# Optimization experiments

Hardware: AMD Instinct MI355X
Metric: run time of the kernel (lower is better)

The kernel has to match this reference:

```python
import jax, jax.numpy as jnp
import numpy as np

N, L, DS, DP, H, A, Q, V = 1, 512, 384, 256, 12, 16, 4, 8
SHID = H * (DP + A + 3 * V + V)  # 3648
WC = float(np.sqrt(2.0 / (9.0 * Q)))
WL = float(np.sqrt(1.0 / 3.0))
EPS = 1e-5


def quat2rot(q):
    # q: (..., 3) partial quaternion (w fixed to 1, then normalized) -> (..., 3, 3)
    ones = jnp.ones(q.shape[:-1] + (1,), q.dtype)
    qf = jnp.concatenate([ones, q], axis=-1)
    qf = qf / jnp.linalg.norm(qf, axis=-1, keepdims=True)
    w, x, y, z = qf[..., 0], qf[..., 1], qf[..., 2], qf[..., 3]
    r0 = jnp.stack([1 - 2 * (y * y + z * z), 2 * (x * y - w * z), 2 * (x * z + w * y)], -1)
    r1 = jnp.stack([2 * (x * y + w * z), 1 - 2 * (x * x + z * z), 2 * (y * z - w * x)], -1)
    r2 = jnp.stack([2 * (x * z - w * y), 2 * (y * z + w * x), 1 - 2 * (x * x + y * y)], -1)
    return jnp.stack([r0, r1, r2], axis=-2)


def layer_norm(x, g, b):
    m = x.mean(-1, keepdims=True)
    v = ((x - m) ** 2).mean(-1, keepdims=True)
    return (x - m) / jnp.sqrt(v + EPS) * g + b


def setup_inputs() -> dict:
    key = jax.random.key(0)
    ks = jax.random.split(key, 24)
    w = lambda k, shape, s=0.02: (jax.random.normal(k, shape, jnp.float32) * s)
    return {
        'sfea': jax.random.normal(ks[0], (N, L, DS), jnp.float32),
        'pfea': jax.random.normal(ks[1], (N, L, L, DP), jnp.float32),
        'quat': jax.random.normal(ks[2], (N, L, 3), jnp.float32) * 0.1,
        'trsl': jax.random.normal(ks[3], (N, L, 3), jnp.float32),
        'Wq': w(ks[4], (DS, H * A)), 'Wk': w(ks[5], (DS, H * A)), 'Wv': w(ks[6], (DS, H * A)),
        'Wqp': w(ks[7], (DS, H * Q * 3)), 'Wkp': w(ks[8], (DS, H * Q * 3)), 'Wvp': w(ks[9], (DS, H * V * 3)),
        'Wb': w(ks[10], (DP, H)),
        'scale': jnp.ones((H,), jnp.float32),
        'Ws': w(ks[11], (SHID, DS)), 'bs': jnp.zeros((DS,), jnp.float32),
        'W1': w(ks[12], (DS, DS)), 'b1': jnp.zeros((DS,), jnp.float32),
        'W2': w(ks[13], (DS, DS)), 'b2': jnp.zeros((DS,), jnp.float32),
        'W3': w(ks[14], (DS, DS)), 'b3': jnp.zeros((DS,), jnp.float32),
        'g1': jnp.ones((DS,), jnp.float32), 'be1': jnp.zeros((DS,), jnp.float32),
        'g2': jnp.ones((DS,), jnp.float32), 'be2': jnp.zeros((DS,), jnp.float32),
    }


def reference(sfea, pfea, quat, trsl, Wq, Wk, Wv, Wqp, Wkp, Wvp, Wb, scale, Ws, bs,
              W1, b1, W2, b2, W3, b3, g1, be1, g2, be2):
    n, l = sfea.shape[0], sfea.shape[1]
    # projections
    q = (sfea @ Wq).reshape(n, l, H, A)
    k = (sfea @ Wk).reshape(n, l, H, A)
    v = (sfea @ Wv).reshape(n, l, H, A)
    qp = (sfea @ Wqp).reshape(n, l, H, Q, 3)
    kp = (sfea @ Wkp).reshape(n, l, H, Q, 3)
    vp = (sfea @ Wvp).reshape(n, l, H, V, 3)
    b = jnp.einsum('nijp,ph->nijh', pfea, Wb)
    # local frames
    rot = quat2rot(quat)  # (n, l, 3, 3)
    t = trsl[:, :, None, None, :]
    qp_g = jnp.einsum('nlij,nlhqj->nlhqi', rot, qp) + t
    kp_g = jnp.einsum('nlij,nlhqj->nlhqi', rot, kp) + t
    vp_g = jnp.einsum('nlij,nlhvj->nlhvi', rot, vp) + t
    # attention logits
    qk = jnp.einsum('nihd,njhd->nijh', q, k) / np.sqrt(A)
    diff = qp_g[:, :, None] - kp_g[:, None]  # (n, i, j, h, q, 3)
    d2 = jnp.sum(diff * diff, axis=(-1, -2))  # (n, i, j, h)
    qkp = (WC * jax.nn.softplus(scale) / 2.0) * d2
    a = jax.nn.softmax(WL * (qk + b - qkp), axis=2)  # (n, i, j, h)
    # weighted sums (einsum avoids huge broadcast intermediates)
    op = jnp.einsum('nijh,nijp->nihp', a, pfea)
    ov = jnp.einsum('nijh,njhd->nihd', a, v)
    ovp_g = jnp.einsum('nijh,njhvc->nihvc', a, vp_g)
    # map back into local frame: R^T (x - t)
    ovp = jnp.einsum('nlji,nlhvj->nlhvi', rot, ovp_g - t)
    ovp_norm = jnp.sqrt(jnp.sum(ovp * ovp, axis=-1))  # (n, l, h, v)
    shid = jnp.concatenate([op, ov, ovp.reshape(n, l, H, V * 3), ovp_norm], axis=-1)
    shid = shid.reshape(n, l, SHID)
    # output projection + residual, post-LN, MLP, post-LN (v1 path, p_drop=0)
    s = sfea + shid @ Ws + bs
    s = layer_norm(s, g1, be1)
    h = jax.nn.relu(s @ W1 + b1)
    h = jax.nn.relu(h @ W2 + b2)
    s = s + (h @ W3 + b3)
    s = layer_norm(s, g2, be2)
    return s
```

## Files before the change

### kernel.cpp

```cpp
#include <hip/hip_runtime.h>
#include <cstddef>

typedef __attribute__((ext_vector_type(8))) short short8;
typedef __attribute__((ext_vector_type(4))) float f32x4;

#define WC_CONST 0.2357022603955158f
#define WL_CONST 0.5773502691896258f

__device__ __forceinline__ unsigned short rne_bf16(float f) {
  unsigned int u = __float_as_uint(f);
  u += 0x7fffu + ((u >> 16) & 1u);
  return (unsigned short)(u >> 16);
}

__global__ __launch_bounds__(256) void concat_w_kernel(
    const float* __restrict__ Wq, const float* __restrict__ Wk, const float* __restrict__ Wv,
    const float* __restrict__ Wqp, const float* __restrict__ Wkp, const float* __restrict__ Wvp,
    float* __restrict__ Wcat) {
  int idx = blockIdx.x * 256 + threadIdx.x;
  if (idx >= 384 * 1152) return;
  int k = idx / 1152, c = idx % 1152;
  float v;
  if (c < 192)       v = Wq [k*192 + c];
  else if (c < 384)  v = Wk [k*192 + (c-192)];
  else if (c < 576)  v = Wv [k*192 + (c-384)];
  else if (c < 720)  v = Wqp[k*144 + (c-576)];
  else if (c < 864)  v = Wkp[k*144 + (c-720)];
  else               v = Wvp[k*288 + (c-864)];
  Wcat[idx] = v;
}

__global__ __launch_bounds__(256) void gemm64_kernel(
    const float* __restrict__ Amat, const float* __restrict__ Bmat, float* __restrict__ Cp,
    int M, int N, int K, int ksl) {
  __shared__ float As[16][68];
  __shared__ float Bs[16][68];
  int t = threadIdx.x;
  int bn = blockIdx.x, bm = blockIdx.y, bz = blockIdx.z;
  int k0 = bz * ksl;
  int tr = t >> 4, tc = t & 15;
  int lm = t >> 2, lk4 = (t & 3) << 2;
  int lkb = t >> 4, lnq = (t & 15) << 2;
  const float* Ab = Amat + (size_t)(bm*64 + lm) * K;
  const float* Bb = Bmat + bn*64 + lnq;
  float acc[4][4];
  #pragma unroll
  for (int a2 = 0; a2 < 4; a2++)
    #pragma unroll
    for (int b2 = 0; b2 < 4; b2++) acc[a2][b2] = 0.f;

  for (int k = k0; k < k0 + ksl; k += 16) {
    float4 av = *(const float4*)(Ab + k + lk4);
    float4 bv = *(const float4*)(Bb + (size_t)(k + lkb) * N);
    As[lk4+0][lm] = av.x; As[lk4+1][lm] = av.y; As[lk4+2][lm] = av.z; As[lk4+3][lm] = av.w;
    *(float4*)&Bs[lkb][lnq] = bv;
    __syncthreads();
    #pragma unroll
    for (int kk = 0; kk < 16; kk++) {
      float4 a4 = *(const float4*)&As[kk][tr << 2];
      float4 b4 = *(const float4*)&Bs[kk][tc << 2];
      float ar[4] = {a4.x, a4.y, a4.z, a4.w};
      float br[4] = {b4.x, b4.y, b4.z, b4.w};
      #pragma unroll
      for (int a2 = 0; a2 < 4; a2++)
        #pragma unroll
        for (int b2 = 0; b2 < 4; b2++) acc[a2][b2] += ar[a2] * br[b2];
    }
    __syncthreads();
  }
  float* Cb = Cp + (size_t)bz * M * N + (size_t)(bm*64 + (tr << 2)) * N + bn*64 + (tc << 2);
  #pragma unroll
  for (int r = 0; r < 4; r++) {
    float4 o = {acc[r][0], acc[r][1], acc[r][2], acc[r][3]};
    *(float4*)(Cb + (size_t)r * N) = o;
  }
}

__global__ __launch_bounds__(256) void reduce_kernel(
    const float* __restrict__ Cp, float* __restrict__ out, const float* __restrict__ bias,
    int relu, int MN, int N, int sk) {
  int idx = blockIdx.x * 256 + threadIdx.x;
  if (idx >= MN) return;
  float s = 0.f;
  for (int z = 0; z < sk; z++) s += Cp[(size_t)z * MN + idx];
  if (bias) s += bias[idx % N];
  if (relu) s = fmaxf(s, 0.f);
  out[idx] = s;
}

__global__ __launch_bounds__(256) void gemm32_kernel(
    const float* __restrict__ Amat, const float* __restrict__ Bmat,
    const float* __restrict__ bias,
    float* __restrict__ C, int M, int N, int K, int relu) {
  __shared__ float As[16][34];
  __shared__ float Bs[16][34];
  int t = threadIdx.x;
  int bn = blockIdx.x, bm = blockIdx.y;
  int tr = t >> 4, tc = t & 15;
  int lm = t >> 3, lk2 = (t & 7) << 1;
  int lkb = t >> 4, ln2 = (t & 15) << 1;
  const float* Ab = Amat + (size_t)(bm*32 + lm) * K;
  const float* Bb = Bmat + bn*32 + ln2;
  float a00=0.f, a01=0.f, a10=0.f, a11=0.f;
  for (int k = 0; k < K; k += 16) {
    float2 av = *(const float2*)(Ab + k + lk2);
    float2 bv = *(const float2*)(Bb + (size_t)(k + lkb) * N);
    As[lk2][lm] = av.x; As[lk2+1][lm] = av.y;
    *(float2*)&Bs[lkb][ln2] = bv;
    __syncthreads();
    #pragma unroll
    for (int kk = 0; kk < 16; kk++) {
      float2 a2 = *(const float2*)&As[kk][tr << 1];
      float2 b2 = *(const float2*)&Bs[kk][tc << 1];
      a00 += a2.x*b2.x; a01 += a2.x*b2.y; a10 += a2.y*b2.x; a11 += a2.y*b2.y;
    }
    __syncthreads();
  }
  int r0 = bm*32 + (tr << 1), c0 = bn*32 + (tc << 1);
  float bb0 = bias ? bias[c0] : 0.f, bb1 = bias ? bias[c0+1] : 0.f;
  float o00 = a00 + bb0, o01 = a01 + bb1, o10 = a10 + bb0, o11 = a11 + bb1;
  if (relu) { o00=fmaxf(o00,0.f); o01=fmaxf(o01,0.f); o10=fmaxf(o10,0.f); o11=fmaxf(o11,0.f); }
  float2 w0 = {o00, o01}, w1 = {o10, o11};
  *(float2*)(C + (size_t)r0*N + c0) = w0;
  *(float2*)(C + (size_t)(r0+1)*N + c0) = w1;
}

__global__ __launch_bounds__(64) void frames_kernel(
    const float* __restrict__ proj, const float* __restrict__ quat, const float* __restrict__ trsl,
    float* __restrict__ rotb, float* __restrict__ qpg, float* __restrict__ kpg,
    float* __restrict__ vpg) {
  int i = blockIdx.x, t = threadIdx.x;
  float q0 = quat[i*3+0], q1 = quat[i*3+1], q2 = quat[i*3+2];
  float inv = rsqrtf(1.f + q0*q0 + q1*q1 + q2*q2);
  float w = inv, x = q0*inv, y = q1*inv, z = q2*inv;
  float R00 = 1.f - 2.f*(y*y + z*z), R01 = 2.f*(x*y - w*z), R02 = 2.f*(x*z + w*y);
  float R10 = 2.f*(x*y + w*z), R11 = 1.f - 2.f*(x*x + z*z), R12 = 2.f*(y*z - w*x);
  float R20 = 2.f*(x*z - w*y), R21 = 2.f*(y*z + w*x), R22 = 1.f - 2.f*(x*x + y*y);
  float t0 = trsl[i*3+0], t1 = trsl[i*3+1], t2 = trsl[i*3+2];
  if (t == 0) {
    float* rb = rotb + i*9;
    rb[0]=R00; rb[1]=R01; rb[2]=R02; rb[3]=R10; rb[4]=R11; rb[5]=R12; rb[6]=R20; rb[7]=R21; rb[8]=R22;
  }
  for (int pt = t; pt < 192; pt += 64) {
    const float* src; float* dst;
    if (pt < 48)      { src = proj + i*1152 + 576 + pt*3;        dst = qpg + i*144 + pt*3; }
    else if (pt < 96) { src = proj + i*1152 + 720 + (pt-48)*3;   dst = kpg + i*144 + (pt-48)*3; }
    else              { src = proj + i*1152 + 864 + (pt-96)*3;   dst = vpg + i*288 + (pt-96)*3; }
    float p0 = src[0], p1 = src[1], p2 = src[2];
    dst[0] = R00*p0 + R01*p1 + R02*p2 + t0;
    dst[1] = R10*p0 + R11*p1 + R12*p2 + t1;
    dst[2] = R20*p0 + R21*p1 + R22*p2 + t2;
  }
}

__global__ __launch_bounds__(256) void bgemm_kernel(
    const float* __restrict__ pfea, const float* __restrict__ Wb, float* __restrict__ bmat) {
  __shared__ short wbf[8][64][8];
  int t = threadIdx.x;
  for (int s = t; s < 512; s += 256) {
    int ks = s >> 6, l = s & 63;
    int col = l & 15, kb = ks * 32 + ((l >> 4) << 3);
    #pragma unroll
    for (int j = 0; j < 8; j++)
      wbf[ks][l][j] = (col < 12) ? (short)rne_bf16(Wb[(kb + j) * 12 + col]) : (short)0;
  }
  __syncthreads();
  int wv = t >> 6, lane = t & 63;
  int wglob = blockIdx.x * 4 + wv;
  int row = lane & 15, kq = lane >> 4;
  for (int it = 0; it < 4; it++) {
    int tile = wglob * 4 + it;
    size_t p0 = (size_t)tile * 16;
    const float* Ab = pfea + (p0 + row) * 256 + kq * 8;
    f32x4 acc = {0.f, 0.f, 0.f, 0.f};
    #pragma unroll
    for (int ks = 0; ks < 8; ks++) {
      float4 f0 = *(const float4*)(Ab + ks * 32);
      float4 f1 = *(const float4*)(Ab + ks * 32 + 4);
      short8 af;
      af[0] = (short)rne_bf16(f0.x); af[1] = (short)rne_bf16(f0.y);
      af[2] = (short)rne_bf16(f0.z); af[3] = (short)rne_bf16(f0.w);
      af[4] = (short)rne_bf16(f1.x); af[5] = (short)rne_bf16(f1.y);
      af[6] = (short)rne_bf16(f1.z); af[7] = (short)rne_bf16(f1.w);
      short8 bfv = *(const short8*)(&wbf[ks][lane][0]);
      acc = __builtin_amdgcn_mfma_f32_16x16x32_bf16(af, bfv, acc, 0, 0, 0);
    }
    int col = lane & 15;
    if (col < 12) {
      #pragma unroll
      for (int r = 0; r < 4; r++) {
        size_t pr = p0 + kq * 4 + r;
        bmat[pr * 12 + col] = acc[r];
      }
    }
  }
}

__device__ __forceinline__ float lt1_val(
    const float* __restrict__ proj, const float* __restrict__ kpg,
    const float* qs_, const float* qps_, float coef, int jg, int h) {
  const float4* kr = (const float4*)(proj + (size_t)jg*1152 + 192 + h*16);
  const float4* qr = (const float4*)(qs_ + h*16);
  float qk = 0.f;
  #pragma unroll
  for (int m = 0; m < 4; m++) {
    float4 kv = kr[m], qv = qr[m];
    qk += qv.x*kv.x + qv.y*kv.y + qv.z*kv.z + qv.w*kv.w;
  }
  const float4* kpr = (const float4*)(kpg + (size_t)jg*144 + h*12);
  const float4* qpr = (const float4*)(qps_ + h*12);
  float d2 = 0.f;
  #pragma unroll
  for (int m = 0; m < 3; m++) {
    float4 kv = kpr[m], qv = qpr[m];
    float dx = qv.x-kv.x, dy = qv.y-kv.y, dz = qv.z-kv.z, dw = qv.w-kv.w;
    d2 += dx*dx + dy*dy + dz*dz + dw*dw;
  }
  return qk*0.25f - coef*d2;
}

__global__ __launch_bounds__(768) void attn5_kernel(
    const float* __restrict__ proj, const float* __restrict__ qpg,
    const float* __restrict__ kpg, const float* __restrict__ vpg,
    const float* __restrict__ pfea, const float* __restrict__ bmat,
    const float* __restrict__ rotb, const float* __restrict__ trsl,
    const float* __restrict__ scale, float* __restrict__ shid) {
  __shared__ float Lws[512][12];
  __shared__ __align__(16) float4 opred[12][2][64];
  __shared__ __align__(16) float qs[12][16];
  __shared__ __align__(16) float qps[12][12];
  __shared__ float coefs[12], sh_inv[12], rot_s[9];
  __shared__ float ovpg_l[12][24];

  int i = blockIdx.x, t = threadIdx.x;
  int w = t >> 6, lane = t & 63;

  for (int idx = t; idx < 192; idx += 768) qs[idx >> 4][idx & 15] = proj[i*1152 + idx];
  for (int idx = t; idx < 144; idx += 768) qps[idx / 12][idx % 12] = qpg[i*144 + idx];
  if (t < 12) coefs[t] = WC_CONST * 0.5f * log1pf(__expf(scale[t]));
  if (t < 9)  rot_s[t] = rotb[i*9 + t];
  __syncthreads();

  #pragma unroll
  for (int r = 0; r < 8; r++) {
    int idx = t + r * 768;
    int j = idx / 12, h = idx - j * 12;
    float lb = lt1_val(proj, kpg, &qs[0][0], &qps[0][0], coefs[h], j, h);
    Lws[j][h] = __expf(WL_CONST * (lb + bmat[(size_t)i * 6144 + idx]));
  }
  __syncthreads();

  {
    float sacc = 0.f;
    #pragma unroll
    for (int r2 = 0; r2 < 8; r2++) sacc += Lws[lane + 64 * r2][w];
    #pragma unroll
    for (int off = 32; off >= 1; off >>= 1) sacc += __shfl_xor(sacc, off);
    if (lane == 0) sh_inv[w] = 1.0f / sacc;
  }

  float4 opacc[12];
  #pragma unroll
  for (int h = 0; h < 12; h++) { opacc[h].x=0.f; opacc[h].y=0.f; opacc[h].z=0.f; opacc[h].w=0.f; }
  float accv[3] = {0.f, 0.f, 0.f};
  float accvp[5] = {0.f, 0.f, 0.f, 0.f, 0.f};
  int hv0 = lane >> 4, hv1 = 4 + (lane >> 4), hv2 = 8 + (lane >> 4);
  int hp0 = lane / 24, hp1 = (lane + 64) / 24, hp2 = (lane + 128) / 24,
      hp3 = (lane + 192) / 24, hp4 = (lane + 256) / 24;

  const float* pf = pfea + (size_t)i * 131072 + (lane << 2);
  int nrows = (w < 8) ? 43 : 42;

  float4 pv0 = *(const float4*)(pf + (size_t)w * 256);
  float4 pv1 = *(const float4*)(pf + (size_t)(w + 12) * 256);

  for (int r = 0; r < nrows; r++) {
    int j = w + 12 * r;
    float4 pv = pv0;
    pv0 = pv1;
    int jn = w + 12 * (r + 2); if (jn > 511) jn = 511;
    pv1 = *(const float4*)(pf + (size_t)jn * 256);

    const float* vrow  = proj + (size_t)j * 1152 + 384 + lane;
    const float* vprow = vpg  + (size_t)j * 288 + lane;
    float vv0 = vrow[0],  vv1 = vrow[64],  vv2 = vrow[128];
    float vp0 = vprow[0], vp1 = vprow[64], vp2 = vprow[128], vp3 = vprow[192];
    float vp4 = (lane < 32) ? vprow[256] : 0.f;

    const float4* lwp = (const float4*)&Lws[j][0];
    float4 lw0 = lwp[0], lw1 = lwp[1], lw2 = lwp[2];
    float wv[12] = {lw0.x, lw0.y, lw0.z, lw0.w,
                    lw1.x, lw1.y, lw1.z, lw1.w,
                    lw2.x, lw2.y, lw2.z, lw2.w};
    #pragma unroll
    for (int h = 0; h < 12; h++) {
      opacc[h].x += wv[h] * pv.x; opacc[h].y += wv[h] * pv.y;
      opacc[h].z += wv[h] * pv.z; opacc[h].w += wv[h] * pv.w;
    }
    accv[0] += wv[hv0] * vv0; accv[1] += wv[hv1] * vv1; accv[2] += wv[hv2] * vv2;
    accvp[0] += wv[hp0] * vp0; accvp[1] += wv[hp1] * vp1;
    accvp[2] += wv[hp2] * vp2; accvp[3] += wv[hp3] * vp3;
    if (lane < 32) accvp[4] += wv[hp4] * vp4;
  }
  __syncthreads();

  #pragma unroll
  for (int g = 0; g < 6; g++) {
    opred[w][0][lane] = opacc[2*g + 0];
    opred[w][1][lane] = opacc[2*g + 1];
    __syncthreads();
    if (t < 128) {
      int hh = t >> 6, ll = t & 63;
      float4 s = {0.f, 0.f, 0.f, 0.f};
      #pragma unroll
      for (int w2 = 0; w2 < 12; w2++) {
        float4 v = opred[w2][hh][ll];
        s.x += v.x; s.y += v.y; s.z += v.z; s.w += v.w;
      }
      int h = 2*g + hh;
      float isv = sh_inv[h];
      float4 o = {s.x*isv, s.y*isv, s.z*isv, s.w*isv};
      *(float4*)(shid + (size_t)i * 3648 + h * 304 + (ll << 2)) = o;
    }
    __syncthreads();
  }

  float* fred = (float*)&opred[0][0][0];
  fred[w * 192 + lane]       = accv[0];
  fred[w * 192 + 64 + lane]  = accv[1];
  fred[w * 192 + 128 + lane] = accv[2];
  __syncthreads();
  if (t < 192) {
    int h = t >> 4;
    float s = 0.f;
    #pragma unroll
    for (int w2 = 0; w2 < 12; w2++) s += fred[w2 * 192 + t];
    shid[(size_t)i * 3648 + h * 304 + 256 + (t & 15)] = s * sh_inv[h];
  }
  __syncthreads();

  #pragma unroll
  for (int k = 0; k < 4; k++) fred[w * 288 + 64 * k + lane] = accvp[k];
  if (lane < 32) fred[w * 288 + 256 + lane] = accvp[4];
  __syncthreads();
  if (t < 288) {
    int h = t / 24;
    float s = 0.f;
    #pragma unroll
    for (int w2 = 0; w2 < 12; w2++) s += fred[w2 * 288 + t];
    ovpg_l[h][t - h * 24] = s * sh_inv[h];
  }
  __syncthreads();

  if (t < 96) {
    int h = t >> 3, vv = t & 7;
    float x = ovpg_l[h][vv*3+0] - trsl[i*3+0];
    float y = ovpg_l[h][vv*3+1] - trsl[i*3+1];
    float z = ovpg_l[h][vv*3+2] - trsl[i*3+2];
    float o0 = rot_s[0]*x + rot_s[3]*y + rot_s[6]*z;
    float o1 = rot_s[1]*x + rot_s[4]*y + rot_s[7]*z;
    float o2 = rot_s[2]*x + rot_s[5]*y + rot_s[8]*z;
    float* so = shid + (size_t)i*3648 + h*304 + 272 + vv*3;
    so[0] = o0; so[1] = o1; so[2] = o2;
    shid[(size_t)i*3648 + h*304 + 296 + vv] = sqrtf(o0*o0 + o1*o1 + o2*o2);
  }
}

__global__ __launch_bounds__(384) void ln384_kernel(
    const float* __restrict__ resid, const float* __restrict__ C, const float* __restrict__ bias,
    const float* __restrict__ g, const float* __restrict__ be, float* __restrict__ out) {
  int i = blockIdx.x, t = threadIdx.x;
  __shared__ float red[6];
  float x = resid[(size_t)i*384 + t] + C[(size_t)i*384 + t] + bias[t];
  float s = x;
  #pragma unroll
  for (int off = 32; off >= 1; off >>= 1) s += __shfl_xor(s, off);
  if ((t & 63) == 0) red[t >> 6] = s;
  __syncthreads();
  float m = (red[0]+red[1]+red[2]+red[3]+red[4]+red[5]) * (1.f/384.f);
  __syncthreads();
  float d = x - m;
  float v = d * d;
  #pragma unroll
  for (int off = 32; off >= 1; off >>= 1) v += __shfl_xor(v, off);
  if ((t & 63) == 0) red[t >> 6] = v;
  __syncthreads();
  float var = (red[0]+red[1]+red[2]+red[3]+red[4]+red[5]) * (1.f/384.f);
  out[(size_t)i*384 + t] = d * rsqrtf(var + 1e-5f) * g[t] + be[t];
}

extern "C" void kernel_launch(void* const* d_in, const int* in_sizes, int n_in,
                              void* d_out, int out_size, void* d_ws, size_t ws_size,
                              hipStream_t stream) {
  const float* sfea = (const float*)d_in[0];
  const float* pfea = (const float*)d_in[1];
  const float* quat = (const float*)d_in[2];
  const float* trsl = (const float*)d_in[3];
  const float* Wq   = (const float*)d_in[4];
  const float* Wk   = (const float*)d_in[5];
  const float* Wv   = (const float*)d_in[6];
  const float* Wqp  = (const float*)d_in[7];
  const float* Wkp  = (const float*)d_in[8];
  const float* Wvp  = (const float*)d_in[9];
  const float* Wb   = (const float*)d_in[10];
  const float* scale= (const float*)d_in[11];
  const float* Wsm  = (const float*)d_in[12];
  const float* bs   = (const float*)d_in[13];
  const float* W1   = (const float*)d_in[14];
  const float* b1   = (const float*)d_in[15];
  const float* W2   = (const float*)d_in[16];
  const float* b2   = (const float*)d_in[17];
  const float* W3   = (const float*)d_in[18];
  const float* b3   = (const float*)d_in[19];
  const float* g1   = (const float*)d_in[20];
  const float* be1  = (const float*)d_in[21];
  const float* g2   = (const float*)d_in[22];
  const float* be2  = (const float*)d_in[23];
  float* out = (float*)d_out;
  float* wsf = (float*)d_ws;

  float* Wcat = wsf;
  float* proj = Wcat + 442368;
  float* rotb = proj + 589824;
  float* qpg  = rotb + 4608;
  float* kpg  = qpg + 73728;
  float* vpg  = kpg + 73728;
  float* bmat = vpg + 147456;
  float* shid = bmat + 3145728;
  float* cpart= shid + 1867776;
  float* C1   = cpart + 1179648;
  float* s1   = C1 + 196608;
  float* h1   = s1 + 196608;
  float* h2   = h1 + 196608;
  float* C3   = h2 + 196608;

  concat_w_kernel<<<1728, 256, 0, stream>>>(Wq, Wk, Wv, Wqp, Wkp, Wvp, Wcat);
  gemm64_kernel<<<dim3(18, 8, 1), 256, 0, stream>>>(sfea, Wcat, proj, 512, 1152, 384, 384);
  frames_kernel<<<512, 64, 0, stream>>>(proj, quat, trsl, rotb, qpg, kpg, vpg);
  bgemm_kernel<<<1024, 256, 0, stream>>>(pfea, Wb, bmat);
  attn5_kernel<<<512, 768, 0, stream>>>(proj, qpg, kpg, vpg, pfea, bmat, rotb, trsl, scale, shid);

  gemm64_kernel<<<dim3(6, 8, 6), 256, 0, stream>>>(shid, Wsm, cpart, 512, 384, 3648, 608);
  reduce_kernel<<<768, 256, 0, stream>>>(cpart, C1, nullptr, 0, 196608, 384, 6);
  ln384_kernel<<<512, 384, 0, stream>>>(sfea, C1, bs, g1, be1, s1);

  gemm32_kernel<<<dim3(12, 16), 256, 0, stream>>>(s1, W1, b1, h1, 512, 384, 384, 1);
  gemm32_kernel<<<dim3(12, 16), 256, 0, stream>>>(h1, W2, b2, h2, 512, 384, 384, 1);
  gemm32_kernel<<<dim3(12, 16), 256, 0, stream>>>(h2, W3, nullptr, C3, 512, 384, 384, 0);
  ln384_kernel<<<512, 384, 0, stream>>>(s1, C3, b3, g2, be2, out);
}
```

Before: 332.3 us.

## Widen attention block to 16 waves with contiguous rows and float4 value loads

The attention kernel now runs 1024 threads (16 waves) instead of 768. Each wave walks a contiguous run of 32 key rows rather than a stride-12 interleave. The v and vp gathers change from several scalar loads per row to float4 loads with a two-row-ahead prefetch, and pfea gets a three-row-ahead prefetch. The cross-wave reductions widen to 16 partials and use float4 stores. This aims to raise memory-level parallelism and cut load instruction count, at the cost of more shared memory for partials. The launch-bounds hint of 4 blocks per CU may push the compiler to limit registers and spill the 48-float accumulator set.

```diff
diff --git a/kernel.cpp b/kernel.cpp
--- a/kernel.cpp
+++ b/kernel.cpp
@@ -219,14 +219,14 @@
   return qk*0.25f - coef*d2;
 }
 
-__global__ __launch_bounds__(768) void attn5_kernel(
+__global__ __launch_bounds__(1024, 4) void attn6_kernel(
     const float* __restrict__ proj, const float* __restrict__ qpg,
     const float* __restrict__ kpg, const float* __restrict__ vpg,
     const float* __restrict__ pfea, const float* __restrict__ bmat,
     const float* __restrict__ rotb, const float* __restrict__ trsl,
     const float* __restrict__ scale, float* __restrict__ shid) {
   __shared__ float Lws[512][12];
-  __shared__ __align__(16) float4 opred[12][2][64];
+  __shared__ __align__(16) float4 opred[16][2][64];
   __shared__ __align__(16) float qs[12][16];
   __shared__ __align__(16) float qps[12][12];
   __shared__ float coefs[12], sh_inv[12], rot_s[9];
@@ -235,22 +235,22 @@
   int i = blockIdx.x, t = threadIdx.x;
   int w = t >> 6, lane = t & 63;
 
-  for (int idx = t; idx < 192; idx += 768) qs[idx >> 4][idx & 15] = proj[i*1152 + idx];
-  for (int idx = t; idx < 144; idx += 768) qps[idx / 12][idx % 12] = qpg[i*144 + idx];
+  for (int idx = t; idx < 192; idx += 1024) qs[idx >> 4][idx & 15] = proj[i*1152 + idx];
+  for (int idx = t; idx < 144; idx += 1024) qps[idx / 12][idx % 12] = qpg[i*144 + idx];
   if (t < 12) coefs[t] = WC_CONST * 0.5f * log1pf(__expf(scale[t]));
   if (t < 9)  rot_s[t] = rotb[i*9 + t];
   __syncthreads();
 
   #pragma unroll
-  for (int r = 0; r < 8; r++) {
-    int idx = t + r * 768;
+  for (int r = 0; r < 6; r++) {
+    int idx = t + r * 1024;
     int j = idx / 12, h = idx - j * 12;
     float lb = lt1_val(proj, kpg, &qs[0][0], &qps[0][0], coefs[h], j, h);
     Lws[j][h] = __expf(WL_CONST * (lb + bmat[(size_t)i * 6144 + idx]));
   }
   __syncthreads();
 
-  {
+  if (w < 12) {
     float sacc = 0.f;
     #pragma unroll
     for (int r2 = 0; r2 < 8; r2++) sacc += Lws[lane + 64 * r2][w];
@@ -262,30 +262,40 @@
   float4 opacc[12];
   #pragma unroll
   for (int h = 0; h < 12; h++) { opacc[h].x=0.f; opacc[h].y=0.f; opacc[h].z=0.f; opacc[h].w=0.f; }
-  float accv[3] = {0.f, 0.f, 0.f};
-  float accvp[5] = {0.f, 0.f, 0.f, 0.f, 0.f};
-  int hv0 = lane >> 4, hv1 = 4 + (lane >> 4), hv2 = 8 + (lane >> 4);
-  int hp0 = lane / 24, hp1 = (lane + 64) / 24, hp2 = (lane + 128) / 24,
-      hp3 = (lane + 192) / 24, hp4 = (lane + 256) / 24;
-
-  const float* pf = pfea + (size_t)i * 131072 + (lane << 2);
-  int nrows = (w < 8) ? 43 : 42;
-
-  float4 pv0 = *(const float4*)(pf + (size_t)w * 256);
-  float4 pv1 = *(const float4*)(pf + (size_t)(w + 12) * 256);
-
-  for (int r = 0; r < nrows; r++) {
-    int j = w + 12 * r;
-    float4 pv = pv0;
-    pv0 = pv1;
-    int jn = w + 12 * (r + 2); if (jn > 511) jn = 511;
-    pv1 = *(const float4*)(pf + (size_t)jn * 256);
-
-    const float* vrow  = proj + (size_t)j * 1152 + 384 + lane;
-    const float* vprow = vpg  + (size_t)j * 288 + lane;
-    float vv0 = vrow[0],  vv1 = vrow[64],  vv2 = vrow[128];
-    float vp0 = vprow[0], vp1 = vprow[64], vp2 = vprow[128], vp3 = vprow[192];
-    float vp4 = (lane < 32) ? vprow[256] : 0.f;
+  float4 accv  = {0.f, 0.f, 0.f, 0.f};
+  float4 accvp = {0.f, 0.f, 0.f, 0.f};
+  float4 accvt = {0.f, 0.f, 0.f, 0.f};
+  int hva = (lane < 48) ? (lane >> 2) : 0;
+  int hpa = lane / 6;
+  int hpt = (lane < 2) ? 10 : 11;
+
+  int j0 = w * 32;
+  const float* pfp  = pfea + (size_t)i * 131072 + (size_t)j0 * 256 + (lane << 2);
+  const float* vbp  = proj + (size_t)j0 * 1152 + 384 + (lane << 2);
+  const float* vpbp = vpg  + (size_t)j0 * 288 + (lane << 2);
+  const float* vptp = vpg  + (size_t)j0 * 288 + 256 + (lane << 2);
+
+  float4 pvA = *(const float4*)(pfp);
+  float4 pvB = *(const float4*)(pfp + 256);
+  float4 pvC = *(const float4*)(pfp + 512);
+  float4 vA  = *(const float4*)(vbp);
+  float4 vB  = *(const float4*)(vbp + 1152);
+  float4 vpA = *(const float4*)(vpbp);
+  float4 vpB = *(const float4*)(vpbp + 288);
+  float4 vtA = (lane < 8) ? *(const float4*)(vptp)       : float4{0,0,0,0};
+  float4 vtB = (lane < 8) ? *(const float4*)(vptp + 288) : float4{0,0,0,0};
+
+  for (int r = 0; r < 32; r++) {
+    int j = j0 + r;
+    float4 pv = pvA, vv = vA, vp = vpA, vt = vtA;
+    pvA = pvB; pvB = pvC;
+    int rp3 = (r + 3 < 32) ? (r + 3) : 31;
+    pvC = *(const float4*)(pfp + (size_t)rp3 * 256);
+    vA = vB; vpA = vpB; vtA = vtB;
+    int rp2 = (r + 2 < 32) ? (r + 2) : 31;
+    vB  = *(const float4*)(vbp  + (size_t)rp2 * 1152);
+    vpB = *(const float4*)(vpbp + (size_t)rp2 * 288);
+    if (lane < 8) vtB = *(const float4*)(vptp + (size_t)rp2 * 288);
 
     const float4* lwp = (const float4*)&Lws[j][0];
     float4 lw0 = lwp[0], lw1 = lwp[1], lw2 = lwp[2];
@@ -297,10 +307,12 @@
       opacc[h].x += wv[h] * pv.x; opacc[h].y += wv[h] * pv.y;
       opacc[h].z += wv[h] * pv.z; opacc[h].w += wv[h] * pv.w;
     }
-    accv[0] += wv[hv0] * vv0; accv[1] += wv[hv1] * vv1; accv[2] += wv[hv2] * vv2;
-    accvp[0] += wv[hp0] * vp0; accvp[1] += wv[hp1] * vp1;
-    accvp[2] += wv[hp2] * vp2; accvp[3] += wv[hp3] * vp3;
-    if (lane < 32) accvp[4] += wv[hp4] * vp4;
+    float wva = wv[hva];
+    accv.x += wva * vv.x; accv.y += wva * vv.y; accv.z += wva * vv.z; accv.w += wva * vv.w;
+    float wvp = wv[hpa];
+    accvp.x += wvp * vp.x; accvp.y += wvp * vp.y; accvp.z += wvp * vp.z; accvp.w += wvp * vp.w;
+    float wvt = wv[hpt];
+    accvt.x += wvt * vt.x; accvt.y += wvt * vt.y; accvt.z += wvt * vt.z; accvt.w += wvt * vt.w;
   }
   __syncthreads();
 
@@ -313,7 +325,7 @@
       int hh = t >> 6, ll = t & 63;
       float4 s = {0.f, 0.f, 0.f, 0.f};
       #pragma unroll
-      for (int w2 = 0; w2 < 12; w2++) {
+      for (int w2 = 0; w2 < 16; w2++) {
         float4 v = opred[w2][hh][ll];
         s.x += v.x; s.y += v.y; s.z += v.z; s.w += v.w;
       }
@@ -326,28 +338,26 @@
   }
 
   float* fred = (float*)&opred[0][0][0];
-  fred[w * 192 + lane]       = accv[0];
-  fred[w * 192 + 64 + lane]  = accv[1];
-  fred[w * 192 + 128 + lane] = accv[2];
+  float4* fred4 = (float4*)fred;
+  if (lane < 48) fred4[w * 48 + lane] = accv;
   __syncthreads();
   if (t < 192) {
     int h = t >> 4;
     float s = 0.f;
     #pragma unroll
-    for (int w2 = 0; w2 < 12; w2++) s += fred[w2 * 192 + t];
+    for (int w2 = 0; w2 < 16; w2++) s += fred[w2 * 192 + t];
     shid[(size_t)i * 3648 + h * 304 + 256 + (t & 15)] = s * sh_inv[h];
   }
   __syncthreads();
 
-  #pragma unroll
-  for (int k = 0; k < 4; k++) fred[w * 288 + 64 * k + lane] = accvp[k];
-  if (lane < 32) fred[w * 288 + 256 + lane] = accvp[4];
+  fred4[w * 72 + lane] = accvp;
+  if (lane < 8) fred4[w * 72 + 64 + lane] = accvt;
   __syncthreads();
   if (t < 288) {
     int h = t / 24;
     float s = 0.f;
     #pragma unroll
-    for (int w2 = 0; w2 < 12; w2++) s += fred[w2 * 288 + t];
+    for (int w2 = 0; w2 < 16; w2++) s += fred[w2 * 288 + t];
     ovpg_l[h][t - h * 24] = s * sh_inv[h];
   }
   __syncthreads();
@@ -438,7 +448,7 @@
   gemm64_kernel<<<dim3(18, 8, 1), 256, 0, stream>>>(sfea, Wcat, proj, 512, 1152, 384, 384);
   frames_kernel<<<512, 64, 0, stream>>>(proj, quat, trsl, rotb, qpg, kpg, vpg);
   bgemm_kernel<<<1024, 256, 0, stream>>>(pfea, Wb, bmat);
-  attn5_kernel<<<512, 768, 0, stream>>>(proj, qpg, kpg, vpg, pfea, bmat, rotb, trsl, scale, shid);
+  attn6_kernel<<<512, 1024, 0, stream>>>(proj, qpg, kpg, vpg, pfea, bmat, rotb, trsl, scale, shid);
 
   gemm64_kernel<<<dim3(6, 8, 6), 256, 0, stream>>>(shid, Wsm, cpart, 512, 384, 3648, 608);
   reduce_kernel<<<768, 256, 0, stream>>>(cpart, C1, nullptr, 0, 196608, 384, 6);
```

Result: slower. 385.7 us (+16.1%).

## Split value aggregation into separate kernel with transposed weight and value layouts

Applied to the files above, without the earlier changes.

The attention kernel now only computes softmax weights and the pfea-weighted sum, with each wave pair handling half the heads over a strided set of rows. The per-head weights are written out in a transposed layout. A new kernel computes the v and vp weighted sums as coalesced dot products over transposed value arrays, then applies the inverse frame transform. The bias matrix is also stored transposed so each wave reads its head contiguously. This cuts register pressure and scattered loads in the main loop, at the cost of an extra launch and a roughly 12 MB weight round trip through memory.

```diff
diff --git a/kernel.cpp b/kernel.cpp
--- a/kernel.cpp
+++ b/kernel.cpp
@@ -128,7 +128,7 @@
 __global__ __launch_bounds__(64) void frames_kernel(
     const float* __restrict__ proj, const float* __restrict__ quat, const float* __restrict__ trsl,
     float* __restrict__ rotb, float* __restrict__ qpg, float* __restrict__ kpg,
-    float* __restrict__ vpg) {
+    float* __restrict__ vvT) {
   int i = blockIdx.x, t = threadIdx.x;
   float q0 = quat[i*3+0], q1 = quat[i*3+1], q2 = quat[i*3+2];
   float inv = rsqrtf(1.f + q0*q0 + q1*q1 + q2*q2);
@@ -141,20 +141,34 @@
     float* rb = rotb + i*9;
     rb[0]=R00; rb[1]=R01; rb[2]=R02; rb[3]=R10; rb[4]=R11; rb[5]=R12; rb[6]=R20; rb[7]=R21; rb[8]=R22;
   }
-  for (int pt = t; pt < 192; pt += 64) {
+  for (int pt = t; pt < 96; pt += 64) {
     const float* src; float* dst;
-    if (pt < 48)      { src = proj + i*1152 + 576 + pt*3;        dst = qpg + i*144 + pt*3; }
-    else if (pt < 96) { src = proj + i*1152 + 720 + (pt-48)*3;   dst = kpg + i*144 + (pt-48)*3; }
-    else              { src = proj + i*1152 + 864 + (pt-96)*3;   dst = vpg + i*288 + (pt-96)*3; }
+    if (pt < 48) { src = proj + i*1152 + 576 + pt*3;      dst = qpg + i*144 + pt*3; }
+    else         { src = proj + i*1152 + 720 + (pt-48)*3; dst = kpg + i*144 + (pt-48)*3; }
     float p0 = src[0], p1 = src[1], p2 = src[2];
     dst[0] = R00*p0 + R01*p1 + R02*p2 + t0;
     dst[1] = R10*p0 + R11*p1 + R12*p2 + t1;
     dst[2] = R20*p0 + R21*p1 + R22*p2 + t2;
   }
+  for (int o = t; o < 480; o += 64) {
+    float val;
+    if (o < 192) {
+      val = proj[i*1152 + 384 + o];
+    } else {
+      int m = o - 192;
+      int vi = m / 3, c = m - vi * 3;
+      const float* p = proj + i*1152 + 864 + vi*3;
+      float p0 = p[0], p1 = p[1], p2 = p[2];
+      val = (c == 0) ? (R00*p0 + R01*p1 + R02*p2 + t0)
+          : (c == 1) ? (R10*p0 + R11*p1 + R12*p2 + t1)
+                     : (R20*p0 + R21*p1 + R22*p2 + t2);
+    }
+    vvT[(size_t)o * 512 + i] = val;
+  }
 }
 
 __global__ __launch_bounds__(256) void bgemm_kernel(
-    const float* __restrict__ pfea, const float* __restrict__ Wb, float* __restrict__ bmat) {
+    const float* __restrict__ pfea, const float* __restrict__ Wb, float* __restrict__ bmatT) {
   __shared__ short wbf[8][64][8];
   int t = threadIdx.x;
   for (int s = t; s < 512; s += 256) {
@@ -190,7 +204,7 @@
       #pragma unroll
       for (int r = 0; r < 4; r++) {
         size_t pr = p0 + kq * 4 + r;
-        bmat[pr * 12 + col] = acc[r];
+        bmatT[(pr >> 9) * 6144 + (size_t)col * 512 + (pr & 511)] = acc[r];
       }
     }
   }
@@ -219,18 +233,16 @@
   return qk*0.25f - coef*d2;
 }
 
-__global__ __launch_bounds__(768) void attn5_kernel(
+__global__ __launch_bounds__(768) void attn7_kernel(
     const float* __restrict__ proj, const float* __restrict__ qpg,
-    const float* __restrict__ kpg, const float* __restrict__ vpg,
-    const float* __restrict__ pfea, const float* __restrict__ bmat,
-    const float* __restrict__ rotb, const float* __restrict__ trsl,
-    const float* __restrict__ scale, float* __restrict__ shid) {
+    const float* __restrict__ kpg, const float* __restrict__ pfea,
+    const float* __restrict__ bmatT, const float* __restrict__ scale,
+    float* __restrict__ shid, float* __restrict__ wmatT, float* __restrict__ shinv_g) {
   __shared__ float Lws[512][12];
-  __shared__ __align__(16) float4 opred[12][2][64];
+  __shared__ __align__(16) float4 opred[12][64];
   __shared__ __align__(16) float qs[12][16];
   __shared__ __align__(16) float qps[12][12];
-  __shared__ float coefs[12], sh_inv[12], rot_s[9];
-  __shared__ float ovpg_l[12][24];
+  __shared__ float coefs[12], sh_inv[12];
 
   int i = blockIdx.x, t = threadIdx.x;
   int w = t >> 6, lane = t & 63;
@@ -238,117 +250,120 @@
   for (int idx = t; idx < 192; idx += 768) qs[idx >> 4][idx & 15] = proj[i*1152 + idx];
   for (int idx = t; idx < 144; idx += 768) qps[idx / 12][idx % 12] = qpg[i*144 + idx];
   if (t < 12) coefs[t] = WC_CONST * 0.5f * log1pf(__expf(scale[t]));
-  if (t < 9)  rot_s[t] = rotb[i*9 + t];
-  __syncthreads();
-
-  #pragma unroll
-  for (int r = 0; r < 8; r++) {
-    int idx = t + r * 768;
-    int j = idx / 12, h = idx - j * 12;
-    float lb = lt1_val(proj, kpg, &qs[0][0], &qps[0][0], coefs[h], j, h);
-    Lws[j][h] = __expf(WL_CONST * (lb + bmat[(size_t)i * 6144 + idx]));
-  }
-  __syncthreads();
-
+  __syncthreads();
+
+  float wvals[8];
+  {
+    const float* bT = bmatT + (size_t)i * 6144 + (size_t)w * 512;
+    float* wT = wmatT + (size_t)i * 6144 + (size_t)w * 512;
+    float cf = coefs[w];
+    #pragma unroll
+    for (int r = 0; r < 8; r++) {
+      int j = lane + 64 * r;
+      float lb = lt1_val(proj, kpg, &qs[0][0], &qps[0][0], cf, j, w);
+      float val = __expf(WL_CONST * (lb + bT[j]));
+      Lws[j][w] = val;
+      wT[j] = val;
+      wvals[r] = val;
+    }
+  }
   {
     float sacc = 0.f;
     #pragma unroll
-    for (int r2 = 0; r2 < 8; r2++) sacc += Lws[lane + 64 * r2][w];
+    for (int r = 0; r < 8; r++) sacc += wvals[r];
     #pragma unroll
     for (int off = 32; off >= 1; off >>= 1) sacc += __shfl_xor(sacc, off);
-    if (lane == 0) sh_inv[w] = 1.0f / sacc;
-  }
-
-  float4 opacc[12];
-  #pragma unroll
-  for (int h = 0; h < 12; h++) { opacc[h].x=0.f; opacc[h].y=0.f; opacc[h].z=0.f; opacc[h].w=0.f; }
-  float accv[3] = {0.f, 0.f, 0.f};
-  float accvp[5] = {0.f, 0.f, 0.f, 0.f, 0.f};
-  int hv0 = lane >> 4, hv1 = 4 + (lane >> 4), hv2 = 8 + (lane >> 4);
-  int hp0 = lane / 24, hp1 = (lane + 64) / 24, hp2 = (lane + 128) / 24,
-      hp3 = (lane + 192) / 24, hp4 = (lane + 256) / 24;
-
+    if (lane == 0) { sh_inv[w] = 1.0f / sacc; shinv_g[i*12 + w] = 1.0f / sacc; }
+  }
+  __syncthreads();
+
+  int wp = w >> 1, half = w & 1;
+  int nr = (wp < 2) ? 86 : 85;
+  int off0 = half ? 4 : 0, off1 = half ? 8 : 4;
   const float* pf = pfea + (size_t)i * 131072 + (lane << 2);
-  int nrows = (w < 8) ? 43 : 42;
-
-  float4 pv0 = *(const float4*)(pf + (size_t)w * 256);
-  float4 pv1 = *(const float4*)(pf + (size_t)(w + 12) * 256);
-
-  for (int r = 0; r < nrows; r++) {
-    int j = w + 12 * r;
-    float4 pv = pv0;
-    pv0 = pv1;
-    int jn = w + 12 * (r + 2); if (jn > 511) jn = 511;
-    pv1 = *(const float4*)(pf + (size_t)jn * 256);
-
-    const float* vrow  = proj + (size_t)j * 1152 + 384 + lane;
-    const float* vprow = vpg  + (size_t)j * 288 + lane;
-    float vv0 = vrow[0],  vv1 = vrow[64],  vv2 = vrow[128];
-    float vp0 = vprow[0], vp1 = vprow[64], vp2 = vprow[128], vp3 = vprow[192];
-    float vp4 = (lane < 32) ? vprow[256] : 0.f;
-
-    const float4* lwp = (const float4*)&Lws[j][0];
-    float4 lw0 = lwp[0], lw1 = lwp[1], lw2 = lwp[2];
-    float wv[12] = {lw0.x, lw0.y, lw0.z, lw0.w,
-                    lw1.x, lw1.y, lw1.z, lw1.w,
-                    lw2.x, lw2.y, lw2.z, lw2.w};
-    #pragma unroll
-    for (int h = 0; h < 12; h++) {
-      opacc[h].x += wv[h] * pv.x; opacc[h].y += wv[h] * pv.y;
-      opacc[h].z += wv[h] * pv.z; opacc[h].w += wv[h] * pv.w;
-    }
-    accv[0] += wv[hv0] * vv0; accv[1] += wv[hv1] * vv1; accv[2] += wv[hv2] * vv2;
-    accvp[0] += wv[hp0] * vp0; accvp[1] += wv[hp1] * vp1;
-    accvp[2] += wv[hp2] * vp2; accvp[3] += wv[hp3] * vp3;
-    if (lane < 32) accvp[4] += wv[hp4] * vp4;
+
+  float4 opacc[6];
+  #pragma unroll
+  for (int c = 0; c < 6; c++) { opacc[c].x=0.f; opacc[c].y=0.f; opacc[c].z=0.f; opacc[c].w=0.f; }
+
+  float4 pvA = *(const float4*)(pf + (size_t)wp * 256);
+  float4 pvB = *(const float4*)(pf + (size_t)(wp + 6) * 256);
+  float4 pvC = *(const float4*)(pf + (size_t)(wp + 12) * 256);
+  float4 lwA0 = *(const float4*)&Lws[wp][off0];
+  float4 lwA1 = *(const float4*)&Lws[wp][off1];
+
+  for (int r = 0; r < nr; r++) {
+    float4 pv = pvA;
+    pvA = pvB; pvB = pvC;
+    int jn = wp + 6 * (r + 3); if (jn > 511) jn = 511;
+    pvC = *(const float4*)(pf + (size_t)jn * 256);
+
+    float4 lw0 = lwA0, lw1 = lwA1;
+    int jl = wp + 6 * (r + 1); if (jl > 511) jl = wp;
+    lwA0 = *(const float4*)&Lws[jl][off0];
+    lwA1 = *(const float4*)&Lws[jl][off1];
+
+    float wv0, wv1, wv2, wv3, wv4, wv5;
+    if (half == 0) { wv0=lw0.x; wv1=lw0.y; wv2=lw0.z; wv3=lw0.w; wv4=lw1.x; wv5=lw1.y; }
+    else           { wv0=lw0.z; wv1=lw0.w; wv2=lw1.x; wv3=lw1.y; wv4=lw1.z; wv5=lw1.w; }
+
+    opacc[0].x += wv0*pv.x; opacc[0].y += wv0*pv.y; opacc[0].z += wv0*pv.z; opacc[0].w += wv0*pv.w;
+    opacc[1].x += wv1*pv.x; opacc[1].y += wv1*pv.y; opacc[1].z += wv1*pv.z; opacc[1].w += wv1*pv.w;
+    opacc[2].x += wv2*pv.x; opacc[2].y += wv2*pv.y; opacc[2].z += wv2*pv.z; opacc[2].w += wv2*pv.w;
+    opacc[3].x += wv3*pv.x; opacc[3].y += wv3*pv.y; opacc[3].z += wv3*pv.z; opacc[3].w += wv3*pv.w;
+    opacc[4].x += wv4*pv.x; opacc[4].y += wv4*pv.y; opacc[4].z += wv4*pv.z; opacc[4].w += wv4*pv.w;
+    opacc[5].x += wv5*pv.x; opacc[5].y += wv5*pv.y; opacc[5].z += wv5*pv.z; opacc[5].w += wv5*pv.w;
   }
   __syncthreads();
 
   #pragma unroll
   for (int g = 0; g < 6; g++) {
-    opred[w][0][lane] = opacc[2*g + 0];
-    opred[w][1][lane] = opacc[2*g + 1];
+    opred[half * 6 + wp][lane] = opacc[g];
     __syncthreads();
     if (t < 128) {
       int hh = t >> 6, ll = t & 63;
       float4 s = {0.f, 0.f, 0.f, 0.f};
       #pragma unroll
-      for (int w2 = 0; w2 < 12; w2++) {
-        float4 v = opred[w2][hh][ll];
+      for (int w2 = 0; w2 < 6; w2++) {
+        float4 v = opred[hh * 6 + w2][ll];
         s.x += v.x; s.y += v.y; s.z += v.z; s.w += v.w;
       }
-      int h = 2*g + hh;
+      int h = g + 6 * hh;
       float isv = sh_inv[h];
       float4 o = {s.x*isv, s.y*isv, s.z*isv, s.w*isv};
       *(float4*)(shid + (size_t)i * 3648 + h * 304 + (ll << 2)) = o;
     }
     __syncthreads();
   }
-
-  float* fred = (float*)&opred[0][0][0];
-  fred[w * 192 + lane]       = accv[0];
-  fred[w * 192 + 64 + lane]  = accv[1];
-  fred[w * 192 + 128 + lane] = accv[2];
-  __syncthreads();
-  if (t < 192) {
-    int h = t >> 4;
-    float s = 0.f;
-    #pragma unroll
-    for (int w2 = 0; w2 < 12; w2++) s += fred[w2 * 192 + t];
-    shid[(size_t)i * 3648 + h * 304 + 256 + (t & 15)] = s * sh_inv[h];
-  }
-  __syncthreads();
-
-  #pragma unroll
-  for (int k = 0; k < 4; k++) fred[w * 288 + 64 * k + lane] = accvp[k];
-  if (lane < 32) fred[w * 288 + 256 + lane] = accvp[4];
-  __syncthreads();
-  if (t < 288) {
-    int h = t / 24;
-    float s = 0.f;
-    #pragma unroll
-    for (int w2 = 0; w2 < 12; w2++) s += fred[w2 * 288 + t];
-    ovpg_l[h][t - h * 24] = s * sh_inv[h];
+}
+
+__global__ __launch_bounds__(512) void ovph_kernel(
+    const float* __restrict__ wmatT, const float* __restrict__ vvT,
+    const float* __restrict__ shinv_g, const float* __restrict__ rotb,
+    const float* __restrict__ trsl, float* __restrict__ shid) {
+  __shared__ float ovpg_l[12][24];
+  __shared__ float sh_inv[12], rot_s[9];
+  int i = blockIdx.x, t = threadIdx.x;
+  int w = t >> 6, lane = t & 63;
+  if (t < 12) sh_inv[t] = shinv_g[i*12 + t];
+  if (t >= 16 && t < 25) rot_s[t - 16] = rotb[i*9 + (t - 16)];
+  __syncthreads();
+
+  const float* wbase = wmatT + (size_t)i * 6144;
+  for (int o = w * 60; o < w * 60 + 60; o++) {
+    int h = (o < 192) ? (o >> 4) : ((o - 192) / 24);
+    const float* wrow = wbase + (size_t)h * 512 + lane;
+    const float* vrow = vvT + (size_t)o * 512 + lane;
+    float acc = 0.f;
+    #pragma unroll
+    for (int k = 0; k < 8; k++) acc += wrow[64*k] * vrow[64*k];
+    #pragma unroll
+    for (int off = 32; off >= 1; off >>= 1) acc += __shfl_xor(acc, off);
+    if (lane == 0) {
+      float val = acc * sh_inv[h];
+      if (o < 192) shid[(size_t)i * 3648 + h * 304 + 256 + (o & 15)] = val;
+      else         ovpg_l[h][(o - 192) - h * 24] = val;
+    }
   }
   __syncthreads();
 
@@ -419,26 +434,30 @@
   float* out = (float*)d_out;
   float* wsf = (float*)d_ws;
 
-  float* Wcat = wsf;
-  float* proj = Wcat + 442368;
-  float* rotb = proj + 589824;
-  float* qpg  = rotb + 4608;
-  float* kpg  = qpg + 73728;
-  float* vpg  = kpg + 73728;
-  float* bmat = vpg + 147456;
-  float* shid = bmat + 3145728;
-  float* cpart= shid + 1867776;
-  float* C1   = cpart + 1179648;
-  float* s1   = C1 + 196608;
-  float* h1   = s1 + 196608;
-  float* h2   = h1 + 196608;
-  float* C3   = h2 + 196608;
+  float* Wcat  = wsf;
+  float* proj  = Wcat + 442368;
+  float* rotb  = proj + 589824;
+  float* qpg   = rotb + 4608;
+  float* kpg   = qpg + 73728;
+  float* vvT   = kpg + 73728;
+  float* big   = vvT + 245760;
+  float* wmatT = big + 3145728;
+  float* shinv = wmatT + 3145728;
+  float* shid  = shinv + 6144;
+  float* C1    = shid + 1867776;
+  float* s1    = C1 + 196608;
+  float* h1    = s1 + 196608;
+  float* h2    = h1 + 196608;
+  float* C3    = h2 + 196608;
+  float* bmatT = big;
+  float* cpart = big;
 
   concat_w_kernel<<<1728, 256, 0, stream>>>(Wq, Wk, Wv, Wqp, Wkp, Wvp, Wcat);
   gemm64_kernel<<<dim3(18, 8, 1), 256, 0, stream>>>(sfea, Wcat, proj, 512, 1152, 384, 384);
-  frames_kernel<<<512, 64, 0, stream>>>(proj, quat, trsl, rotb, qpg, kpg, vpg);
-  bgemm_kernel<<<1024, 256, 0, stream>>>(pfea, Wb, bmat);
-  attn5_kernel<<<512, 768, 0, stream>>>(proj, qpg, kpg, vpg, pfea, bmat, rotb, trsl, scale, shid);
+  frames_kernel<<<512, 64, 0, stream>>>(proj, quat, trsl, rotb, qpg, kpg, vvT);
+  bgemm_kernel<<<1024, 256, 0, stream>>>(pfea, Wb, bmatT);
+  attn7_kernel<<<512, 768, 0, stream>>>(proj, qpg, kpg, pfea, bmatT, scale, shid, wmatT, shinv);
+  ovph_kernel<<<512, 512, 0, stream>>>(wmatT, vvT, shinv, rotb, trsl, shid);
 
   gemm64_kernel<<<dim3(6, 8, 6), 256, 0, stream>>>(shid, Wsm, cpart, 512, 384, 3648, 608);
   reduce_kernel<<<768, 256, 0, stream>>>(cpart, C1, nullptr, 0, 196608, 384, 6);
```

Measured after the change: 358.7 us. +7.9%, slower.
